# Kernel tuning notes

Hardware: AMD Instinct MI355X
Metric: run time of the kernel (lower is better)

The kernel has to match this reference:

```python
import jax, jax.numpy as jnp
import numpy as np

N = 50000
NEG_SLOPE = 0.01  # F.leaky_relu default


def gcn_conv(x, edge_index, edge_weight, W, b):
    """PyG GCNConv: h = x @ W; symmetric-normalized aggregation with self-loops; + bias."""
    n = x.shape[0]
    h = x @ W                                # [N, out]
    src, dst = edge_index[0], edge_index[1]
    # degree includes self-loop weight 1.0 per node
    deg = jax.ops.segment_sum(edge_weight, dst, num_segments=n) + 1.0
    dinv = jax.lax.rsqrt(deg)                # deg >= 1, no zero guard needed
    norm = dinv[src] * edge_weight * dinv[dst]
    agg = jax.ops.segment_sum(norm[:, None] * h[src], dst, num_segments=n)
    agg = agg + (dinv * dinv)[:, None] * h   # self-loop contribution: deg^-1 * h_i
    return agg + b


def setup_inputs() -> dict:
    key = jax.random.key(0)
    ks = jax.random.split(key, 24)
    in_size, hid, out = 256, 64, 32
    E = 800000
    d = {}
    for i, nm in enumerate(["x1", "x2", "x3"]):
        d[nm] = jax.random.normal(ks[i], (N, in_size), dtype=jnp.float32)
    for i, nm in enumerate(["edge_index1", "edge_index2", "edge_index3"]):
        d[nm] = jax.random.randint(ks[3 + i], (2, E), 0, N, dtype=jnp.int32)
    for i, nm in enumerate(["edge_weight1", "edge_weight2", "edge_weight3"]):
        d[nm] = jax.random.uniform(ks[6 + i], (E,), dtype=jnp.float32)
    s_in = 1.0 / np.sqrt(in_size)
    s_h = 1.0 / np.sqrt(hid)
    for i, nm in enumerate(["W1", "W2", "W3"]):
        d[nm] = jax.random.uniform(ks[9 + i], (in_size, hid), minval=-s_in, maxval=s_in, dtype=jnp.float32)
    for i, nm in enumerate(["b1", "b2", "b3"]):
        d[nm] = jax.random.uniform(ks[12 + i], (hid,), minval=-s_in, maxval=s_in, dtype=jnp.float32)
    d["fc_w"] = jax.random.uniform(ks[15], (hid, 1), minval=-s_h, maxval=s_h, dtype=jnp.float32)
    d["fc_b"] = jax.random.uniform(ks[16], (1,), minval=-s_h, maxval=s_h, dtype=jnp.float32)
    for i, nm in enumerate(["W11", "W22", "W33"]):
        d[nm] = jax.random.uniform(ks[17 + i], (hid, out), minval=-s_h, maxval=s_h, dtype=jnp.float32)
    for i, nm in enumerate(["b11", "b22", "b33"]):
        d[nm] = jax.random.uniform(ks[20 + i], (out,), minval=-s_h, maxval=s_h, dtype=jnp.float32)
    return d


def reference(x1, x2, x3, edge_index1, edge_index2, edge_index3,
              edge_weight1, edge_weight2, edge_weight3,
              W1, W2, W3, b1, b2, b3, fc_w, fc_b,
              W11, W22, W33, b11, b22, b33):
    # branch embeddings (dropout is identity in eval mode)
    e1 = jax.nn.relu(gcn_conv(x1, edge_index1, edge_weight1, W1, b1))
    e2 = jax.nn.relu(gcn_conv(x2, edge_index2, edge_weight2, W2, b2))
    e3 = jax.nn.relu(gcn_conv(x3, edge_index3, edge_weight3, W3, b3))
    # attention coefficients
    c1 = jnp.exp(jax.nn.leaky_relu(e1 @ fc_w + fc_b, NEG_SLOPE))  # [N,1]
    c2 = jnp.exp(jax.nn.leaky_relu(e2 @ fc_w + fc_b, NEG_SLOPE))
    c3 = jnp.exp(jax.nn.leaky_relu(e3 @ fc_w + fc_b, NEG_SLOPE))
    cd = c1 + c2 + c3
    coef1, coef2, coef3 = c1 / cd, c2 / cd, c3 / cd
    combined = e1 * coef1 + e2 * coef2 + e3 * coef3
    out1 = gcn_conv(combined, edge_index1, edge_weight1, W11, b11)
    out2 = gcn_conv(combined, edge_index2, edge_weight2, W22, b22)
    out3 = gcn_conv(combined, edge_index3, edge_weight3, W33, b33)
    return (out1 + out2 + out3, coef1, coef2, coef3)
```

## Files before the change

### kernel.cpp

```cpp
#include <hip/hip_runtime.h>
#include <hip/hip_fp16.h>
#include <math.h>

#define NN    50000
#define INF_  256
#define HID   64
#define OUTF  32
#define EE    800000
#define TOTN  (3 * NN)
#define NBKT  196
#define NBIN  (3 * NBKT)
#define CBLK  392
#define NCNT  (3 * CBLK)
#define GB    782
#define NGEMM (3 * GB)
#define MAXB  5120

typedef unsigned long long u64;
typedef unsigned int       u32;
typedef unsigned short     u16;
typedef _Float16           f16;
typedef f16   f16x8 __attribute__((ext_vector_type(8)));
typedef f16   f16x4 __attribute__((ext_vector_type(4)));
typedef float f32x4 __attribute__((ext_vector_type(4)));

__global__ __launch_bounds__(256) void k_prep(
        const float* __restrict__ W1, const float* __restrict__ W2, const float* __restrict__ W3,
        f16* __restrict__ Wt, u32* __restrict__ bin_total) {
    int blk = blockIdx.x, t = threadIdx.x;
    if (blk == 3) {
        for (int i = t; i < NBIN; i += 256) bin_total[i] = 0;
        return;
    }
    const float* W = (blk == 0) ? W1 : (blk == 1) ? W2 : W3;
    f16* wt = Wt + blk * HID * INF_;
    for (int idx = t; idx < INF_ * HID; idx += 256) {
        int k = idx >> 6, c = idx & 63;
        wt[c * INF_ + k] = (f16)W[idx];
    }
}

__global__ __launch_bounds__(256) void k_cntgemm(
        const int* __restrict__ ei1, const int* __restrict__ ei2, const int* __restrict__ ei3,
        u32* __restrict__ bin_total, u32* __restrict__ blockbase,
        const float* __restrict__ x1, const float* __restrict__ x2, const float* __restrict__ x3,
        const f16* __restrict__ Wt, __half* __restrict__ h) {
    __shared__ f16 xl[64][72];
    __shared__ f16 wl[64][72];
    int bid = blockIdx.x;
    int q = bid / 3, r = bid - q * 3;
    int t = threadIdx.x;

    if (r == 2) {
        u32* bins = (u32*)xl;
        int cb  = q;
        int br  = cb / CBLK;
        int blk = cb - br * CBLK;
        const int* ei = (br == 0) ? ei1 : (br == 1) ? ei2 : ei3;
        for (int i = t; i < NBKT; i += 256) bins[i] = 0;
        __syncthreads();
        int e0 = blk * 2048;
#pragma unroll
        for (int k = 0; k < 8; ++k) {
            int e = e0 + k * 256 + t;
            if (e < EE) atomicAdd(&bins[(u32)ei[EE + e] >> 8], 1u);
        }
        __syncthreads();
        for (int i = t; i < NBKT; i += 256) {
            u32 c = bins[i];
            u32 base = atomicAdd(&bin_total[br * NBKT + i], c);
            blockbase[cb * NBKT + i] = base;
        }
        return;
    }

    int gid = q * 2 + r;
    if (gid >= NGEMM) return;
    int b = gid / GB;
    int row_base = (gid - b * GB) * 64;
    const float4* x4 = reinterpret_cast<const float4*>((b == 0) ? x1 : (b == 1) ? x2 : x3);
    const f16* wt = Wt + b * HID * INF_;
    __half* hb = h + (size_t)b * NN * HID;

    int w    = t >> 6;
    int lane = t & 63;
    int lrow = lane & 15;
    int lk   = (lane >> 4) * 8;

    f32x4 acc[4] = {{0,0,0,0},{0,0,0,0},{0,0,0,0},{0,0,0,0}};
    for (int kt = 0; kt < 4; ++kt) {
#pragma unroll
        for (int j = 0; j < 4; ++j) {
            int flat = t + j * 256;
            int rr = flat >> 4, c4 = flat & 15;
            int gr = row_base + rr;
            float4 v = (gr < NN) ? x4[(size_t)gr * 64 + kt * 16 + c4]
                                 : make_float4(0.f, 0.f, 0.f, 0.f);
            f16x4 p = {(f16)v.x, (f16)v.y, (f16)v.z, (f16)v.w};
            *(f16x4*)&xl[rr][c4 * 4] = p;
        }
#pragma unroll
        for (int j = 0; j < 2; ++j) {
            int flat = t + j * 256;
            int col = flat >> 3, ko = (flat & 7) * 8;
            *(f16x8*)&wl[col][ko] = *(const f16x8*)&wt[col * INF_ + kt * 64 + ko];
        }
        __syncthreads();
        int arow = (w << 4) + lrow;
        f16x8 a0 = *(const f16x8*)&xl[arow][lk];
        f16x8 a1 = *(const f16x8*)&xl[arow][32 + lk];
#pragma unroll
        for (int c = 0; c < 4; ++c) {
            f16x8 b0 = *(const f16x8*)&wl[c * 16 + lrow][lk];
            f16x8 b1 = *(const f16x8*)&wl[c * 16 + lrow][32 + lk];
            acc[c] = __builtin_amdgcn_mfma_f32_16x16x32_f16(a0, b0, acc[c], 0, 0, 0);
            acc[c] = __builtin_amdgcn_mfma_f32_16x16x32_f16(a1, b1, acc[c], 0, 0, 0);
        }
        __syncthreads();
    }
    int orow0 = row_base + (w << 4) + ((lane >> 4) << 2);
#pragma unroll
    for (int c = 0; c < 4; ++c) {
#pragma unroll
        for (int i = 0; i < 4; ++i) {
            int row = orow0 + i;
            if (row < NN) hb[(size_t)row * HID + c * 16 + lrow] = __float2half(acc[c][i]);
        }
    }
}

__global__ __launch_bounds__(256) void k_scan(const u32* __restrict__ bin_total,
                                              u32* __restrict__ binstart) {
    __shared__ u32 s[256];
    int t = threadIdx.x;
    u32 c[3]; u32 sum = 0;
#pragma unroll
    for (int k = 0; k < 3; ++k) {
        int i = t * 3 + k;
        c[k] = (i < NBIN) ? bin_total[i] : 0;
        sum += c[k];
    }
    s[t] = sum;
    __syncthreads();
    for (int d = 1; d < 256; d <<= 1) {
        u32 v = (t >= d) ? s[t - d] : 0;
        __syncthreads();
        s[t] += v;
        __syncthreads();
    }
    u32 run = s[t] - sum;
#pragma unroll
    for (int k = 0; k < 3; ++k) {
        int i = t * 3 + k;
        if (i < NBIN) binstart[i] = run;
        run += c[k];
    }
    if (t == 255) binstart[NBIN] = run;
}

__global__ __launch_bounds__(256) void k_scatter(
        const int* __restrict__ ei1, const int* __restrict__ ei2, const int* __restrict__ ei3,
        const float* __restrict__ ew1, const float* __restrict__ ew2, const float* __restrict__ ew3,
        const u32* __restrict__ binstart, const u32* __restrict__ blockbase,
        u64* __restrict__ bucketed) {
    __shared__ u32 cur[NBKT];
    int cb  = blockIdx.x;
    int br  = cb / CBLK;
    int blk = cb - br * CBLK;
    const int*   ei = (br == 0) ? ei1 : (br == 1) ? ei2 : ei3;
    const float* ew = (br == 0) ? ew1 : (br == 1) ? ew2 : ew3;
    int t = threadIdx.x;
    for (int i = t; i < NBKT; i += 256) cur[i] = 0;
    __syncthreads();
    int e0 = blk * 2048;
#pragma unroll
    for (int k = 0; k < 8; ++k) {
        int e = e0 + k * 256 + t;
        if (e < EE) {
            u32 dst = (u32)ei[EE + e];
            u32 src = (u32)ei[e];
            u32 bkt = dst >> 8;
            u32 rnk = atomicAdd(&cur[bkt], 1u);
            u32 pos = binstart[br * NBKT + bkt] + blockbase[cb * NBKT + bkt] + rnk;
            bucketed[pos] = ((u64)__float_as_uint(ew[e]) << 32) | (src << 8) | (dst & 0xffu);
        }
    }
}

__global__ __launch_bounds__(256) void k_bucket(
        const u64* __restrict__ bucketed, const u32* __restrict__ bin_total,
        const u32* __restrict__ binstart,
        u32* __restrict__ nodeinfo, float* __restrict__ dinv,
        u32* __restrict__ csr, __half* __restrict__ h) {
    __shared__ u32   scnt[256];
    __shared__ float swsum[256];
    __shared__ u32   scur[256];
    __shared__ u32   sscan[256];
    __shared__ float sdiv[256];
    __shared__ u32   lcsr[MAXB];
    int bin = blockIdx.x;
    int br  = bin / NBKT;
    int bkt = bin - br * NBKT;
    int t = threadIdx.x;
    u32 base = binstart[bin];
    u32 ecnt = bin_total[bin];
    scnt[t] = 0; swsum[t] = 0.f; scur[t] = 0;
    __syncthreads();
    for (u32 i = t; i < ecnt; i += 256) {
        u64 e = bucketed[base + i];
        u32 dl = (u32)e & 0xffu;
        atomicAdd(&scnt[dl], 1u);
        atomicAdd(&swsum[dl], __uint_as_float((u32)(e >> 32)));
    }
    __syncthreads();
    sscan[t] = scnt[t];
    __syncthreads();
    for (int d = 1; d < 256; d <<= 1) {
        u32 v = (t >= d) ? sscan[t - d] : 0;
        __syncthreads();
        sscan[t] += v;
        __syncthreads();
    }
    u32 lstart = sscan[t] - scnt[t];
    float d = rsqrtf(1.0f + swsum[t]);
    sdiv[t] = d;
    int n = bkt * 256 + t;
    if (n < NN) {
        int gi = br * NN + n;
        nodeinfo[gi] = ((base + lstart) << 10) | scnt[t];
        dinv[gi]     = d;
    }
    __syncthreads();
    for (u32 i = t; i < ecnt; i += 256) {
        u64 e = bucketed[base + i];
        u32 dl  = (u32)e & 0xffu;
        u32 src = (u32)(e >> 8) & 0xffffu;
        float w = __uint_as_float((u32)(e >> 32));
        u32 rnk = atomicAdd(&scur[dl], 1u);
        u32 ls  = sscan[dl] - scnt[dl];
        lcsr[ls + rnk] = ((u32)__half_as_ushort(__float2half(w)) << 16) | src;
    }
    __syncthreads();
    for (u32 i = t; i < ecnt; i += 256) csr[base + i] = lcsr[i];

    int nrows = NN - bkt * 256; if (nrows > 256) nrows = 256;
    u32* hrow = (u32*)(h + ((size_t)br * NN + (size_t)bkt * 256) * HID);
    for (int i = t; i < nrows * 32; i += 256) {
        float dd = sdiv[i >> 5];
        __half2 hv = *(__half2*)&hrow[i];
        float2 v = __half22float2(hv);
        __half2 r = __float22half2_rn(make_float2(v.x * dd, v.y * dd));
        hrow[i] = *(u32*)&r;
    }
}

__global__ __launch_bounds__(256) void k_agg_attn(
        const u32* __restrict__ csr, const u32* __restrict__ nodeinfo,
        const float* __restrict__ dinv,
        const float* __restrict__ b1, const float* __restrict__ b2, const float* __restrict__ b3,
        const __half* __restrict__ h,
        const float* __restrict__ fc_w, const float* __restrict__ fc_b,
        __half* __restrict__ comb, float* __restrict__ coef_out) {
    int t   = threadIdx.x;
    int f2  = t & 31;
    int eo  = (t >> 5) & 1;
    int sub = __builtin_amdgcn_readfirstlane(t >> 6);
    int n   = blockIdx.x * 4 + sub;
    float2 wv = ((const float2*)fc_w)[f2];
    float fb = fc_b[0];

    float2 ev[3];
    float c[3];
#pragma unroll
    for (int b = 0; b < 3; ++b) {
        const float* bi = (b == 0) ? b1 : (b == 1) ? b2 : b3;
        const __half2* hb2 = (const __half2*)(h + (size_t)b * NN * HID);
        int i   = b * NN + n;
        u32 inf = nodeinfo[i];
        int cc  = (int)(inf & 1023u);
        int st  = (int)(inf >> 10);
        float d = dinv[i];
        float2 hs = __half22float2(hb2[(size_t)n * 32 + f2]);

        float ax = 0.f, ay = 0.f;
        int cm1 = cc - 1;
        for (int j = 0; j < cc; j += 16) {
            u32 ee[8]; __half2 vv[8];
#pragma unroll
            for (int u = 0; u < 8; ++u) {
                int jj = j + 2 * u + eo;
                ee[u] = csr[st + (jj < cm1 ? jj : cm1)];
                if (jj >= cc) ee[u] &= 0xffffu;
            }
#pragma unroll
            for (int u = 0; u < 8; ++u)
                vv[u] = hb2[(size_t)(ee[u] & 0xffff) * 32 + f2];
#pragma unroll
            for (int u = 0; u < 8; ++u) {
                float w = __half2float(__ushort_as_half((u16)(ee[u] >> 16)));
                float2 v = __half22float2(vv[u]);
                ax = fmaf(w, v.x, ax);
                ay = fmaf(w, v.y, ay);
            }
        }
        ax += __shfl_xor(ax, 32);
        ay += __shfl_xor(ay, 32);
        float2 bv = ((const float2*)bi)[f2];
        float ex = fmaxf(bv.x + d * (hs.x + ax), 0.f);
        float ey = fmaxf(bv.y + d * (hs.y + ay), 0.f);
        ev[b] = make_float2(ex, ey);

        float dd = ex * wv.x + ey * wv.y;
#pragma unroll
        for (int off = 16; off > 0; off >>= 1) dd += __shfl_xor(dd, off);
        float z = dd + fb;
        z = (z > 0.f) ? z : 0.01f * z;
        c[b] = expf(z);
    }
    float cd = c[0] + c[1] + c[2];
    float coef0 = c[0] / cd, coef1 = c[1] / cd, coef2 = c[2] / cd;
    float cx = ev[0].x * coef0 + ev[1].x * coef1 + ev[2].x * coef2;
    float cy = ev[0].y * coef0 + ev[1].y * coef1 + ev[2].y * coef2;
    if (eo == 0)
        ((__half2*)comb)[(size_t)n * 32 + f2] = __float22half2_rn(make_float2(cx, cy));
    if ((t & 63) == 0) {
        coef_out[n]          = coef0;
        coef_out[NN + n]     = coef1;
        coef_out[2 * NN + n] = coef2;
    }
}

__global__ __launch_bounds__(256) void k_gemm2(
        const __half* __restrict__ comb,
        const float* __restrict__ W11, const float* __restrict__ W22, const float* __restrict__ W33,
        const float* __restrict__ dinv, __half* __restrict__ h2) {
    __shared__ float Wls[3][HID][OUTF];
    __shared__ __half cl[8][HID];
    int t = threadIdx.x;
    {
        const float4* w40 = reinterpret_cast<const float4*>(W11);
        const float4* w41 = reinterpret_cast<const float4*>(W22);
        const float4* w42 = reinterpret_cast<const float4*>(W33);
        float4* d0 = reinterpret_cast<float4*>(&Wls[0][0][0]);
        float4* d1 = reinterpret_cast<float4*>(&Wls[1][0][0]);
        float4* d2 = reinterpret_cast<float4*>(&Wls[2][0][0]);
#pragma unroll
        for (int j = 0; j < 2; ++j) {
            d0[t + j * 256] = w40[t + j * 256];
            d1[t + j * 256] = w41[t + j * 256];
            d2[t + j * 256] = w42[t + j * 256];
        }
    }
    int row0 = blockIdx.x * 8;
    ((u32*)cl)[t] = ((const u32*)(comb + (size_t)row0 * HID))[t];
    __syncthreads();

    int col = t & 31;
    int rr  = t >> 5;
    int row = row0 + rr;
    float a0 = 0.f, a1 = 0.f, a2 = 0.f;
    for (int k = 0; k < HID; ++k) {
        float cv = __half2float(cl[rr][k]);
        a0 = fmaf(cv, Wls[0][k][col], a0);
        a1 = fmaf(cv, Wls[1][k][col], a1);
        a2 = fmaf(cv, Wls[2][k][col], a2);
    }
    float d0 = dinv[row], d1 = dinv[NN + row], d2 = dinv[2 * NN + row];
    h2[(size_t)0 * NN * OUTF + (size_t)row * OUTF + col] = __float2half(a0 * d0);
    h2[(size_t)1 * NN * OUTF + (size_t)row * OUTF + col] = __float2half(a1 * d1);
    h2[(size_t)2 * NN * OUTF + (size_t)row * OUTF + col] = __float2half(a2 * d2);
}

__global__ __launch_bounds__(256) void k_agg2(
        const u32* __restrict__ csr, const u32* __restrict__ nodeinfo,
        const float* __restrict__ dinv,
        const float* __restrict__ b11, const float* __restrict__ b22, const float* __restrict__ b33,
        const __half* __restrict__ h2, float* __restrict__ out) {
    int t   = threadIdx.x;
    int f2  = t & 15;
    int eo  = (t >> 4) & 3;
    int sub = __builtin_amdgcn_readfirstlane(t >> 6);
    int n   = blockIdx.x * 4 + sub;

    float2 bA = ((const float2*)b11)[f2];
    float2 bB = ((const float2*)b22)[f2];
    float2 bC = ((const float2*)b33)[f2];
    float tx = bA.x + bB.x + bC.x;
    float ty = bA.y + bB.y + bC.y;
#pragma unroll
    for (int b = 0; b < 3; ++b) {
        int i   = b * NN + n;
        u32 inf = nodeinfo[i];
        int cc  = (int)(inf & 1023u);
        int st  = (int)(inf >> 10);
        const __half2* h2b = (const __half2*)(h2 + (size_t)b * NN * OUTF);
        float ax = 0.f, ay = 0.f;
        int cm1 = cc - 1;
        for (int j = 0; j < cc; j += 16) {
            u32 ee[4]; __half2 vv[4];
#pragma unroll
            for (int u = 0; u < 4; ++u) {
                int jj = j + 4 * u + eo;
                ee[u] = csr[st + (jj < cm1 ? jj : cm1)];
                if (jj >= cc) ee[u] &= 0xffffu;
            }
#pragma unroll
            for (int u = 0; u < 4; ++u)
                vv[u] = h2b[(size_t)(ee[u] & 0xffff) * 16 + f2];
#pragma unroll
            for (int u = 0; u < 4; ++u) {
                float w = __half2float(__ushort_as_half((u16)(ee[u] >> 16)));
                float2 v = __half22float2(vv[u]);
                ax = fmaf(w, v.x, ax);
                ay = fmaf(w, v.y, ay);
            }
        }
        ax += __shfl_xor(ax, 16); ay += __shfl_xor(ay, 16);
        ax += __shfl_xor(ax, 32); ay += __shfl_xor(ay, 32);
        float d = dinv[i];
        float2 hs = __half22float2(h2b[(size_t)n * 16 + f2]);
        tx += d * (ax + hs.x);
        ty += d * (ay + hs.y);
    }
    if (eo == 0)
        ((float2*)out)[(size_t)n * 16 + f2] = make_float2(tx, ty);
}

extern "C" void kernel_launch(void* const* d_in, const int* in_sizes, int n_in,
                              void* d_out, int out_size, void* d_ws, size_t ws_size,
                              hipStream_t stream) {
    const float* x1  = (const float*)d_in[0];
    const float* x2  = (const float*)d_in[1];
    const float* x3  = (const float*)d_in[2];
    const int*   ei1 = (const int*)d_in[3];
    const int*   ei2 = (const int*)d_in[4];
    const int*   ei3 = (const int*)d_in[5];
    const float* ew1 = (const float*)d_in[6];
    const float* ew2 = (const float*)d_in[7];
    const float* ew3 = (const float*)d_in[8];
    const float* W1  = (const float*)d_in[9];
    const float* W2  = (const float*)d_in[10];
    const float* W3  = (const float*)d_in[11];
    const float* b1  = (const float*)d_in[12];
    const float* b2  = (const float*)d_in[13];
    const float* b3  = (const float*)d_in[14];
    const float* fcw = (const float*)d_in[15];
    const float* fcb = (const float*)d_in[16];
    const float* W11 = (const float*)d_in[17];
    const float* W22 = (const float*)d_in[18];
    const float* W33 = (const float*)d_in[19];
    const float* b11 = (const float*)d_in[20];
    const float* b22 = (const float*)d_in[21];
    const float* b33 = (const float*)d_in[22];

    float* out = (float*)d_out;
    float* coef_out = out + (size_t)NN * OUTF;

    u64*   bucketed  = (u64*)d_ws;
    u32*   csr       = (u32*)(bucketed + 3 * EE);
    u32*   bin_total = csr + 3 * EE;
    u32*   binstart  = bin_total + NBIN;
    u32*   blockbase = binstart + NBIN + 4;
    float* dinv      = (float*)(blockbase + NCNT * NBKT);
    u32*   nodeinfo  = (u32*)(dinv + TOTN);
    f16*   Wt        = (f16*)(nodeinfo + TOTN);
    __half* h        = (__half*)(Wt + 3 * HID * INF_);
    __half* comb     = h + (size_t)TOTN * HID;
    __half* h2       = comb + (size_t)NN * HID;

    k_prep<<<dim3(4), 256, 0, stream>>>(W1, W2, W3, Wt, bin_total);
    k_cntgemm<<<dim3(NCNT * 3), 256, 0, stream>>>(ei1, ei2, ei3, bin_total, blockbase,
                                                  x1, x2, x3, Wt, h);
    k_scan<<<dim3(1), 256, 0, stream>>>(bin_total, binstart);
    k_scatter<<<dim3(NCNT), 256, 0, stream>>>(ei1, ei2, ei3, ew1, ew2, ew3,
                                              binstart, blockbase, bucketed);
    k_bucket<<<dim3(NBIN), 256, 0, stream>>>(bucketed, bin_total, binstart,
                                             nodeinfo, dinv, csr, h);

    k_agg_attn<<<dim3(NN / 4), 256, 0, stream>>>(csr, nodeinfo, dinv, b1, b2, b3,
                                                 h, fcw, fcb, comb, coef_out);
    k_gemm2<<<dim3(NN / 8), 256, 0, stream>>>(comb, W11, W22, W33, dinv, h2);
    k_agg2<<<dim3(NN / 4), 256, 0, stream>>>(csr, nodeinfo, dinv,
                                             b11, b22, b33, h2, out);
}
```

Before: 293.9 us.

## Split fused aggregation kernels into per-branch aggregation plus separate attention and sum

The first-layer aggregation+attention kernel is split into a per-branch aggregation kernel (3x the blocks) that writes fp16 embeddings, followed by a lightweight attention/combine kernel. The second-layer aggregation is likewise split per branch into partial outputs in workspace, reduced by a separate sum kernel that adds biases. The aim is more parallelism and better load balance across the three graphs, at the cost of extra global round-trips for intermediates and two more launches.

```diff
diff --git a/kernel.cpp b/kernel.cpp
--- a/kernel.cpp
+++ b/kernel.cpp
@@ -15,6 +15,7 @@
 #define GB    782
 #define NGEMM (3 * GB)
 #define MAXB  5120
+#define NBLK  12500
 
 typedef unsigned long long u64;
 typedef unsigned int       u32;
@@ -254,63 +255,78 @@
     }
 }
 
-__global__ __launch_bounds__(256) void k_agg_attn(
+__global__ __launch_bounds__(256) void k_agg1(
         const u32* __restrict__ csr, const u32* __restrict__ nodeinfo,
         const float* __restrict__ dinv,
         const float* __restrict__ b1, const float* __restrict__ b2, const float* __restrict__ b3,
-        const __half* __restrict__ h,
-        const float* __restrict__ fc_w, const float* __restrict__ fc_b,
-        __half* __restrict__ comb, float* __restrict__ coef_out) {
+        const __half* __restrict__ h, __half* __restrict__ e) {
+    int bid = blockIdx.x;
+    int br  = bid / NBLK;
+    int nb  = bid - br * NBLK;
     int t   = threadIdx.x;
     int f2  = t & 31;
     int eo  = (t >> 5) & 1;
     int sub = __builtin_amdgcn_readfirstlane(t >> 6);
-    int n   = blockIdx.x * 4 + sub;
+    int n   = nb * 4 + sub;
+
+    const float* bi = (br == 0) ? b1 : (br == 1) ? b2 : b3;
+    const __half2* hb2 = (const __half2*)(h + (size_t)br * NN * HID);
+    int i   = br * NN + n;
+    u32 inf = nodeinfo[i];
+    int cc  = (int)(inf & 1023u);
+    int st  = (int)(inf >> 10);
+    float d = dinv[i];
+    float2 hs = __half22float2(hb2[(size_t)n * 32 + f2]);
+
+    float ax = 0.f, ay = 0.f;
+    int cm1 = cc - 1;
+    for (int j = 0; j < cc; j += 16) {
+        u32 ee[8]; __half2 vv[8];
+#pragma unroll
+        for (int u = 0; u < 8; ++u) {
+            int jj = j + 2 * u + eo;
+            ee[u] = csr[st + (jj < cm1 ? jj : cm1)];
+            if (jj >= cc) ee[u] &= 0xffffu;
+        }
+#pragma unroll
+        for (int u = 0; u < 8; ++u)
+            vv[u] = hb2[(size_t)(ee[u] & 0xffff) * 32 + f2];
+#pragma unroll
+        for (int u = 0; u < 8; ++u) {
+            float w = __half2float(__ushort_as_half((u16)(ee[u] >> 16)));
+            float2 v = __half22float2(vv[u]);
+            ax = fmaf(w, v.x, ax);
+            ay = fmaf(w, v.y, ay);
+        }
+    }
+    ax += __shfl_xor(ax, 32);
+    ay += __shfl_xor(ay, 32);
+    float2 bv = ((const float2*)bi)[f2];
+    float ex = fmaxf(bv.x + d * (hs.x + ax), 0.f);
+    float ey = fmaxf(bv.y + d * (hs.y + ay), 0.f);
+    if (eo == 0)
+        ((__half2*)e)[((size_t)br * NN + n) * 32 + f2] = __float22half2_rn(make_float2(ex, ey));
+}
+
+__global__ __launch_bounds__(256) void k_attn(
+        const __half* __restrict__ e,
+        const float* __restrict__ fc_w, const float* __restrict__ fc_b,
+        __half* __restrict__ comb, float* __restrict__ coef_out) {
+    int t    = threadIdx.x;
+    int lane = t & 63;
+    int sub  = __builtin_amdgcn_readfirstlane(t >> 6);
+    int half = lane >> 5;
+    int f2   = lane & 31;
+    int n    = blockIdx.x * 8 + sub * 2 + half;
     float2 wv = ((const float2*)fc_w)[f2];
     float fb = fc_b[0];
-
-    float2 ev[3];
-    float c[3];
+    const __half2* e2 = (const __half2*)e;
+
+    float2 ev[3]; float c[3];
 #pragma unroll
     for (int b = 0; b < 3; ++b) {
-        const float* bi = (b == 0) ? b1 : (b == 1) ? b2 : b3;
-        const __half2* hb2 = (const __half2*)(h + (size_t)b * NN * HID);
-        int i   = b * NN + n;
-        u32 inf = nodeinfo[i];
-        int cc  = (int)(inf & 1023u);
-        int st  = (int)(inf >> 10);
-        float d = dinv[i];
-        float2 hs = __half22float2(hb2[(size_t)n * 32 + f2]);
-
-        float ax = 0.f, ay = 0.f;
-        int cm1 = cc - 1;
-        for (int j = 0; j < cc; j += 16) {
-            u32 ee[8]; __half2 vv[8];
-#pragma unroll
-            for (int u = 0; u < 8; ++u) {
-                int jj = j + 2 * u + eo;
-                ee[u] = csr[st + (jj < cm1 ? jj : cm1)];
-                if (jj >= cc) ee[u] &= 0xffffu;
-            }
-#pragma unroll
-            for (int u = 0; u < 8; ++u)
-                vv[u] = hb2[(size_t)(ee[u] & 0xffff) * 32 + f2];
-#pragma unroll
-            for (int u = 0; u < 8; ++u) {
-                float w = __half2float(__ushort_as_half((u16)(ee[u] >> 16)));
-                float2 v = __half22float2(vv[u]);
-                ax = fmaf(w, v.x, ax);
-                ay = fmaf(w, v.y, ay);
-            }
-        }
-        ax += __shfl_xor(ax, 32);
-        ay += __shfl_xor(ay, 32);
-        float2 bv = ((const float2*)bi)[f2];
-        float ex = fmaxf(bv.x + d * (hs.x + ax), 0.f);
-        float ey = fmaxf(bv.y + d * (hs.y + ay), 0.f);
-        ev[b] = make_float2(ex, ey);
-
-        float dd = ex * wv.x + ey * wv.y;
+        ev[b] = __half22float2(e2[((size_t)b * NN + n) * 32 + f2]);
+        float dd = ev[b].x * wv.x + ev[b].y * wv.y;
 #pragma unroll
         for (int off = 16; off > 0; off >>= 1) dd += __shfl_xor(dd, off);
         float z = dd + fb;
@@ -321,9 +337,8 @@
     float coef0 = c[0] / cd, coef1 = c[1] / cd, coef2 = c[2] / cd;
     float cx = ev[0].x * coef0 + ev[1].x * coef1 + ev[2].x * coef2;
     float cy = ev[0].y * coef0 + ev[1].y * coef1 + ev[2].y * coef2;
-    if (eo == 0)
-        ((__half2*)comb)[(size_t)n * 32 + f2] = __float22half2_rn(make_float2(cx, cy));
-    if ((t & 63) == 0) {
+    ((__half2*)comb)[(size_t)n * 32 + f2] = __float22half2_rn(make_float2(cx, cy));
+    if (f2 == 0) {
         coef_out[n]          = coef0;
         coef_out[NN + n]     = coef1;
         coef_out[2 * NN + n] = coef2;
@@ -371,59 +386,69 @@
     h2[(size_t)2 * NN * OUTF + (size_t)row * OUTF + col] = __float2half(a2 * d2);
 }
 
-__global__ __launch_bounds__(256) void k_agg2(
+__global__ __launch_bounds__(256) void k_agg2p(
         const u32* __restrict__ csr, const u32* __restrict__ nodeinfo,
         const float* __restrict__ dinv,
-        const float* __restrict__ b11, const float* __restrict__ b22, const float* __restrict__ b33,
-        const __half* __restrict__ h2, float* __restrict__ out) {
+        const __half* __restrict__ h2, float* __restrict__ outp) {
+    int bid = blockIdx.x;
+    int br  = bid / NBLK;
+    int nb  = bid - br * NBLK;
     int t   = threadIdx.x;
     int f2  = t & 15;
     int eo  = (t >> 4) & 3;
     int sub = __builtin_amdgcn_readfirstlane(t >> 6);
-    int n   = blockIdx.x * 4 + sub;
-
+    int n   = nb * 4 + sub;
+
+    int i   = br * NN + n;
+    u32 inf = nodeinfo[i];
+    int cc  = (int)(inf & 1023u);
+    int st  = (int)(inf >> 10);
+    const __half2* h2b = (const __half2*)(h2 + (size_t)br * NN * OUTF);
+    float ax = 0.f, ay = 0.f;
+    int cm1 = cc - 1;
+    for (int j = 0; j < cc; j += 16) {
+        u32 ee[4]; __half2 vv[4];
+#pragma unroll
+        for (int u = 0; u < 4; ++u) {
+            int jj = j + 4 * u + eo;
+            ee[u] = csr[st + (jj < cm1 ? jj : cm1)];
+            if (jj >= cc) ee[u] &= 0xffffu;
+        }
+#pragma unroll
+        for (int u = 0; u < 4; ++u)
+            vv[u] = h2b[(size_t)(ee[u] & 0xffff) * 16 + f2];
+#pragma unroll
+        for (int u = 0; u < 4; ++u) {
+            float w = __half2float(__ushort_as_half((u16)(ee[u] >> 16)));
+            float2 v = __half22float2(vv[u]);
+            ax = fmaf(w, v.x, ax);
+            ay = fmaf(w, v.y, ay);
+        }
+    }
+    ax += __shfl_xor(ax, 16); ay += __shfl_xor(ay, 16);
+    ax += __shfl_xor(ax, 32); ay += __shfl_xor(ay, 32);
+    float d = dinv[i];
+    float2 hs = __half22float2(h2b[(size_t)n * 16 + f2]);
+    if (eo == 0)
+        ((float2*)outp)[((size_t)br * NN + n) * 16 + f2] =
+            make_float2(d * (ax + hs.x), d * (ay + hs.y));
+}
+
+__global__ __launch_bounds__(256) void k_sum(
+        const float* __restrict__ outp,
+        const float* __restrict__ b11, const float* __restrict__ b22, const float* __restrict__ b33,
+        float* __restrict__ out) {
+    int i = blockIdx.x * 256 + threadIdx.x;
+    int f2 = i & 15;
+    const float2* p = (const float2*)outp;
+    float2 v0 = p[i];
+    float2 v1 = p[(size_t)NN * 16 + i];
+    float2 v2 = p[(size_t)2 * NN * 16 + i];
     float2 bA = ((const float2*)b11)[f2];
     float2 bB = ((const float2*)b22)[f2];
     float2 bC = ((const float2*)b33)[f2];
-    float tx = bA.x + bB.x + bC.x;
-    float ty = bA.y + bB.y + bC.y;
-#pragma unroll
-    for (int b = 0; b < 3; ++b) {
-        int i   = b * NN + n;
-        u32 inf = nodeinfo[i];
-        int cc  = (int)(inf & 1023u);
-        int st  = (int)(inf >> 10);
-        const __half2* h2b = (const __half2*)(h2 + (size_t)b * NN * OUTF);
-        float ax = 0.f, ay = 0.f;
-        int cm1 = cc - 1;
-        for (int j = 0; j < cc; j += 16) {
-            u32 ee[4]; __half2 vv[4];
-#pragma unroll
-            for (int u = 0; u < 4; ++u) {
-                int jj = j + 4 * u + eo;
-                ee[u] = csr[st + (jj < cm1 ? jj : cm1)];
-                if (jj >= cc) ee[u] &= 0xffffu;
-            }
-#pragma unroll
-            for (int u = 0; u < 4; ++u)
-                vv[u] = h2b[(size_t)(ee[u] & 0xffff) * 16 + f2];
-#pragma unroll
-            for (int u = 0; u < 4; ++u) {
-                float w = __half2float(__ushort_as_half((u16)(ee[u] >> 16)));
-                float2 v = __half22float2(vv[u]);
-                ax = fmaf(w, v.x, ax);
-                ay = fmaf(w, v.y, ay);
-            }
-        }
-        ax += __shfl_xor(ax, 16); ay += __shfl_xor(ay, 16);
-        ax += __shfl_xor(ax, 32); ay += __shfl_xor(ay, 32);
-        float d = dinv[i];
-        float2 hs = __half22float2(h2b[(size_t)n * 16 + f2]);
-        tx += d * (ax + hs.x);
-        ty += d * (ay + hs.y);
-    }
-    if (eo == 0)
-        ((float2*)out)[(size_t)n * 16 + f2] = make_float2(tx, ty);
+    ((float2*)out)[i] = make_float2(v0.x + v1.x + v2.x + bA.x + bB.x + bC.x,
+                                    v0.y + v1.y + v2.y + bA.y + bB.y + bC.y);
 }
 
 extern "C" void kernel_launch(void* const* d_in, const int* in_sizes, int n_in,
@@ -457,6 +482,7 @@
     float* coef_out = out + (size_t)NN * OUTF;
 
     u64*   bucketed  = (u64*)d_ws;
+    float* outp      = (float*)d_ws;
     u32*   csr       = (u32*)(bucketed + 3 * EE);
     u32*   bin_total = csr + 3 * EE;
     u32*   binstart  = bin_total + NBIN;
@@ -467,6 +493,7 @@
     __half* h        = (__half*)(Wt + 3 * HID * INF_);
     __half* comb     = h + (size_t)TOTN * HID;
     __half* h2       = comb + (size_t)NN * HID;
+    __half* e        = h2 + (size_t)TOTN * OUTF;
 
     k_prep<<<dim3(4), 256, 0, stream>>>(W1, W2, W3, Wt, bin_total);
     k_cntgemm<<<dim3(NCNT * 3), 256, 0, stream>>>(ei1, ei2, ei3, bin_total, blockbase,
@@ -477,9 +504,9 @@
     k_bucket<<<dim3(NBIN), 256, 0, stream>>>(bucketed, bin_total, binstart,
                                              nodeinfo, dinv, csr, h);
 
-    k_agg_attn<<<dim3(NN / 4), 256, 0, stream>>>(csr, nodeinfo, dinv, b1, b2, b3,
-                                                 h, fcw, fcb, comb, coef_out);
+    k_agg1<<<dim3(3 * NBLK), 256, 0, stream>>>(csr, nodeinfo, dinv, b1, b2, b3, h, e);
+    k_attn<<<dim3(NN / 8), 256, 0, stream>>>(e, fcw, fcb, comb, coef_out);
     k_gemm2<<<dim3(NN / 8), 256, 0, stream>>>(comb, W11, W22, W33, dinv, h2);
-    k_agg2<<<dim3(NN / 4), 256, 0, stream>>>(csr, nodeinfo, dinv,
-                                             b11, b22, b33, h2, out);
-}
+    k_agg2p<<<dim3(3 * NBLK), 256, 0, stream>>>(csr, nodeinfo, dinv, h2, outp);
+    k_sum<<<dim3(3125), 256, 0, stream>>>(outp, b11, b22, b33, out);
+}
```

Result: no change. 290.7 us (-1.1%).
